# Performance work log

Hardware: AMD Instinct MI355X
Metric: run time of the kernel (lower is better)

The kernel has to match this reference:

```python
import jax, jax.numpy as jnp
import numpy as np

SPANS = [15, 9, 5]   # processed largest-first, matching sorted(span_groups, reverse=True)
DEPTH = 2
TOL = 1.5


def _rmsnorm(x, eps=1e-5):
    return x * jax.lax.rsqrt(jnp.mean(x * x, axis=-1, keepdims=True) + eps)


def _block(m, g, Wi, Wz, Wdt, bdt, alog, Wo, Wyg):
    """Dual-input gated selective-scan block (stand-in for create_multihead_block
    block_type='dual_input'): match stream runs a diagonal SSM scan over window
    tokens, gated by the geometry stream; both streams are residually updated."""
    u = _rmsnorm(m) @ Wi                              # [P,L,C]
    z = jax.nn.silu(_rmsnorm(g) @ Wz)                 # [P,L,C] geom gate
    delta = jax.nn.softplus(u @ Wdt + bdt)            # [P,L,C]
    decay = jnp.exp(delta * (-jnp.exp(alog)))         # [P,L,C]
    x_in = delta * u

    def step(h, inp):
        d, xi = inp
        h = d * h + xi
        return h, h

    _, hs = jax.lax.scan(step, jnp.zeros_like(x_in[:, 0]),
                         (jnp.swapaxes(decay, 0, 1), jnp.swapaxes(x_in, 0, 1)))
    y = jnp.swapaxes(hs, 0, 1) * z                    # [P,L,C]
    return m + y @ Wo, g + jax.nn.silu(y @ Wyg)


def _sample(feat_flat, ys, xs, H, W):
    """Bilinear sampling, align_corners=True, padding_mode='zeros'.
    feat_flat: [C, H*W]; ys, xs: [L] float coords. Returns [L, C]."""
    y0 = jnp.floor(ys); x0 = jnp.floor(xs)
    wy = ys - y0; wx = xs - x0

    def tap(yi, xi):
        valid = ((yi >= 0) & (yi <= H - 1) & (xi >= 0) & (xi <= W - 1)).astype(feat_flat.dtype)
        idx = (jnp.clip(yi, 0, H - 1).astype(jnp.int32) * W
               + jnp.clip(xi, 0, W - 1).astype(jnp.int32))
        return feat_flat[:, idx] * valid              # [C,L]

    v = (tap(y0, x0) * (1 - wy) * (1 - wx) + tap(y0, x0 + 1) * (1 - wy) * wx
         + tap(y0 + 1, x0) * wy * (1 - wx) + tap(y0 + 1, x0 + 1) * wy * wx)
    return v.T


def _process_side(feat_m, feat_g, flow, sx, sy, params):
    B, C, H, W = feat_m.shape
    G = feat_g.shape[1]
    Wi, Wz, Wdt, bdt, alog, Wo, Wyg = params
    dt = feat_m.dtype
    bb, yy, xx = [a.ravel() for a in jnp.meshgrid(jnp.arange(B), jnp.arange(H), jnp.arange(W), indexing='ij')]
    # flow-shifted sub-pixel window centers, clamped (flow[...,0]=dx, flow[...,1]=dy)
    cy = jnp.clip(yy.astype(dt) + flow[bb, yy, xx, 1], 0, H - 1)
    cx = jnp.clip(xx.astype(dt) + flow[bb, yy, xx, 0], 0, W - 1)
    avg = ((sx + sy) * 0.5).ravel()
    assigned = jnp.zeros(avg.shape, dtype=bool)
    fm = feat_m.reshape(B, C, H * W)
    fg = feat_g.reshape(B, G, H * W)
    out_m = jnp.zeros((B * H * W, C), dt)
    out_g = jnp.zeros((B * H * W, G), dt)
    wsum = jnp.zeros((B * H * W,), dt)
    for si, s in enumerate(SPANS):
        # span-group mask; positions claimed by a larger span are excluded
        mask = (jnp.abs(avg - s) < TOL) & (~assigned)
        assigned = assigned | mask
        h = s // 2
        dy, dx = [a.ravel() for a in jnp.meshgrid(jnp.arange(-h, h + 1), jnp.arange(-h, h + 1), indexing='ij')]
        dist = jnp.sqrt((dy * dy + dx * dx).astype(dt))
        pw = jnp.exp(-dist / (s / 2.0))
        pw = pw / pw.sum()                             # normalized distance weights [L]
        ys = cy[:, None] + dy[None, :].astype(dt)      # [P,L]
        xs = cx[:, None] + dx[None, :].astype(dt)
        wm = jax.vmap(lambda b, y, x: _sample(fm[b], y, x, H, W))(bb, ys, xs)  # [P,L,C]
        wg = jax.vmap(lambda b, y, x: _sample(fg[b], y, x, H, W))(bb, ys, xs)  # [P,L,G]
        for d in range(DEPTH):
            wm, wg = _block(wm, wg, Wi[si, d], Wz[si, d], Wdt[si, d], bdt[si, d], alog[si, d], Wo[si, d], Wyg[si, d])
        # scatter-accumulate around the integer center position
        ty = yy[:, None] + dy[None, :]
        tx = xx[:, None] + dx[None, :]
        valid = ((ty >= 0) & (ty < H) & (tx >= 0) & (tx < W)).astype(dt)
        w = pw[None, :] * mask[:, None].astype(dt) * valid           # [P,L]
        idx = bb[:, None] * (H * W) + jnp.clip(ty, 0, H - 1) * W + jnp.clip(tx, 0, W - 1)
        out_m = out_m.at[idx.ravel()].add((wm * w[..., None]).reshape(-1, C))
        out_g = out_g.at[idx.ravel()].add((wg * w[..., None]).reshape(-1, G))
        wsum = wsum.at[idx.ravel()].add(w.ravel())
    ws = jnp.maximum(wsum, 1e-6)[:, None]
    om = (out_m / ws).reshape(B, H, W, C).transpose(0, 3, 1, 2)
    og = (out_g / ws).reshape(B, H, W, G).transpose(0, 3, 1, 2)
    return om, og


def setup_inputs() -> dict:
    key = jax.random.key(0)
    ks = jax.random.split(key, 18)
    B, C, G, H, W = 1, 128, 64, 28, 28
    f32 = jnp.float32
    d = {}
    d['feat_match_0'] = jax.random.normal(ks[0], (B, C, H, W), f32)
    d['feat_match_1'] = jax.random.normal(ks[1], (B, C, H, W), f32)
    d['feat_geom_0'] = jax.random.normal(ks[2], (B, G, H, W), f32)
    d['feat_geom_1'] = jax.random.normal(ks[3], (B, G, H, W), f32)
    d['flow_map_0'] = 1.5 * jax.random.normal(ks[4], (B, H, W, 4), f32)
    d['flow_map_1'] = 1.5 * jax.random.normal(ks[5], (B, H, W, 4), f32)
    # spans in [3, 17) so each span group {5, 9, 15} is populated
    d['adaptive_spans_x_0'] = 3.0 + 14.0 * jax.random.uniform(ks[6], (B, H, W), f32)
    d['adaptive_spans_y_0'] = 3.0 + 14.0 * jax.random.uniform(ks[7], (B, H, W), f32)
    d['adaptive_spans_x_1'] = 3.0 + 14.0 * jax.random.uniform(ks[8], (B, H, W), f32)
    d['adaptive_spans_y_1'] = 3.0 + 14.0 * jax.random.uniform(ks[9], (B, H, W), f32)
    # per-span (order [15,9,5]) x per-depth block parameters
    d['W_in'] = jax.random.normal(ks[10], (3, DEPTH, C, C), f32) / np.sqrt(C).astype(np.float32)
    d['W_z'] = jax.random.normal(ks[11], (3, DEPTH, G, C), f32) / np.sqrt(G).astype(np.float32)
    d['W_dt'] = jax.random.normal(ks[12], (3, DEPTH, C, C), f32) / np.sqrt(C).astype(np.float32)
    d['b_dt'] = 0.1 * jax.random.normal(ks[13], (3, DEPTH, C), f32)
    d['a_log'] = 0.1 * jax.random.normal(ks[14], (3, DEPTH, C), f32)
    d['W_out'] = jax.random.normal(ks[15], (3, DEPTH, C, C), f32) / np.sqrt(C).astype(np.float32)
    d['W_yg'] = jax.random.normal(ks[16], (3, DEPTH, C, G), f32) / np.sqrt(C).astype(np.float32)
    return d


def reference(feat_match_0, feat_match_1, feat_geom_0, feat_geom_1,
              flow_map_0, flow_map_1,
              adaptive_spans_x_0, adaptive_spans_y_0,
              adaptive_spans_x_1, adaptive_spans_y_1,
              W_in, W_z, W_dt, b_dt, a_log, W_out, W_yg):
    params = (W_in, W_z, W_dt, b_dt, a_log, W_out, W_yg)
    m0, g0 = _process_side(feat_match_0, feat_geom_0, flow_map_0[..., :2],
                           adaptive_spans_x_0, adaptive_spans_y_0, params)
    m1, g1 = _process_side(feat_match_1, feat_geom_1, flow_map_1[..., :2],
                           adaptive_spans_x_1, adaptive_spans_y_1, params)
    return m0, m1, g0, g1
```

## Files before the change

### kernel.cpp

```cpp
#include <hip/hip_runtime.h>
#include <math.h>

typedef short s16x8 __attribute__((ext_vector_type(8)));
typedef unsigned short u16x8v __attribute__((ext_vector_type(8)));
typedef float f32x4 __attribute__((ext_vector_type(4)));

#define HH 28
#define WW 28
#define PP 784
#define CC 128
#define GG 64
#define MT 48
#define NH 3
#define AST 136
#define GSTB 72

#define OFF_FMT0 0
#define OFF_FMT1 100352
#define OFF_FGT0 200704
#define OFF_FGT1 250880
#define OFF_ACCM0 301056
#define OFF_ACCM1 401408
#define OFF_ACCG0 501760
#define OFF_ACCG1 551936
#define OFF_ACCW0 602112
#define OFF_ACCW1 602896
#define ACC_FLOATS 302624
#define OFF_CNT   603680
#define OFF_CNT2  603704
#define OFF_JOB   603728
#define OFF_WB    605296

#define WIB 0
#define WZB 98304
#define WDB 147456
#define WOB 245760
#define WYB 344064

struct KArgs {
  const float* fm[2]; const float* fg[2];
  const float* flow[2]; const float* sx[2]; const float* sy[2];
  const float* Wi; const float* Wz; const float* Wdt; const float* bdt;
  const float* alog; const float* Wo; const float* Wyg;
  float* fmT[2]; float* fgT[2];
  float* accm[2]; float* accg[2]; float* accw[2];
  int* cnt; int* cnt2; int* job;
  unsigned short* wb;
  float* out;
};

__device__ __forceinline__ int span_group(float avg, int& s) {
  if (fabsf(avg - 15.f) < 1.5f) { s = 15; return 0; }
  if (fabsf(avg - 9.f)  < 1.5f) { s = 9;  return 1; }
  if (fabsf(avg - 5.f)  < 1.5f) { s = 5;  return 2; }
  s = 0; return 3;
}

__device__ __forceinline__ float fast_silu(float x) {
  return x * __builtin_amdgcn_rcpf(1.f + __expf(-x));
}

__device__ __forceinline__ unsigned short f2bf(float f) {
  unsigned u = __float_as_uint(f);
  unsigned r = (u + 0x7fffu + ((u >> 16) & 1u)) >> 16;
  return (unsigned short)r;
}
__device__ __forceinline__ float b2f(unsigned short u) {
  return __uint_as_float(((unsigned)u) << 16);
}

#define MFMA(A_, B_, C_) __builtin_amdgcn_mfma_f32_16x16x32_bf16((A_), (B_), (C_), 0, 0, 0)

__global__ void k_zero(float* p, int n) {
  int j = blockIdx.x * 256 + threadIdx.x;
  if (j < n) p[j] = 0.f;
}

__global__ void k_prep(KArgs a) {
  int j = blockIdx.x * 256 + threadIdx.x;
  int side = j / 150528; int r = j - side * 150528;
  int p = r / 192; int ch = r - p * 192;
  if (ch < CC) a.fmT[side][p * CC + ch] = a.fm[side][ch * PP + p];
  else         a.fgT[side][p * GG + (ch - CC)] = a.fg[side][(ch - CC) * PP + p];
}

__global__ void k_prepw(KArgs a) {
  int j = blockIdx.x * 256 + threadIdx.x;
  unsigned short* wb = a.wb;
  if (j < 98304) {
    int set = j >> 14, r = j & 16383; int o = r >> 7, c = r & 127;
    wb[WIB + j] = f2bf(a.Wi[set * 16384 + c * 128 + o]);
  } else if (j < 147456) {
    int r = j - 98304; int set = r >> 13, rr = r & 8191; int o = rr >> 6, c = rr & 63;
    wb[WZB + r] = f2bf(a.Wz[set * 8192 + c * 128 + o]);
  } else if (j < 245760) {
  } else if (j < 344064) {
    int r = j - 245760; int set = r >> 14, rr = r & 16383; int o = rr >> 7, c = rr & 127;
    wb[WOB + r] = f2bf(a.Wo[set * 16384 + c * 128 + o]);
  } else {
    int r = j - 344064; int set = r >> 13, rr = r & 8191; int o = rr >> 7, c = rr & 127;
    wb[WYB + r] = f2bf(a.Wyg[set * 8192 + c * 64 + o]);
  }
}

__global__ void k_prepwid(KArgs a) {
  __shared__ float wi_row[128];
  const int set = blockIdx.x, i = blockIdx.y, o = threadIdx.x;
  wi_row[o] = a.Wi[set * 16384 + i * 128 + o];
  __syncthreads();
  float acc = 0.f;
#pragma unroll 4
  for (int m = 0; m < 128; ++m) acc = fmaf(wi_row[m], a.Wdt[set * 16384 + m * 128 + o], acc);
  a.wb[WDB + set * 16384 + o * 128 + i] = f2bf(acc);
}

__global__ void k_count(KArgs a) {
  int j = blockIdx.x * 256 + threadIdx.x;
  if (j >= 2 * PP) return;
  a.job[j] = -1;
  int side = j / PP, p = j - side * PP;
  float avg = 0.5f * (a.sx[side][p] + a.sy[side][p]);
  int s; int g = span_group(avg, s);
  if (g < 3) {
    int py = p / WW, px = p - py * WW;
    int region = (py / 14) * 4 + px / 7;
    atomicAdd(&a.cnt[region * 3 + g], 1);
  }
}

__global__ void k_assign(KArgs a) {
  int j = blockIdx.x * 256 + threadIdx.x;
  if (j >= 2 * PP) return;
  int side = j / PP, p = j - side * PP;
  float avg = 0.5f * (a.sx[side][p] + a.sy[side][p]);
  int s; int g = span_group(avg, s);
  if (g < 3) {
    int py = p / WW, px = p - py * WW;
    int region = (py / 14) * 4 + px / 7;
    int base = 0;
    for (int gg = 0; gg < g; ++gg) base += a.cnt[region * 3 + gg];
    int rank = base + atomicAdd(&a.cnt2[region * 3 + g], 1);
    a.job[region + 8 * rank] = (side << 10) | p;
  }
}

__global__ void k_fin(KArgs a) {
  int j = blockIdx.x * 256 + threadIdx.x;
  int side = j / 150528; int r = j - side * 150528;
  int p = r / 192; int ch = r - p * 192;
  float inv = 1.f / fmaxf(a.accw[side][p], 1e-6f);
  if (ch < CC) a.out[side * 100352 + ch * PP + p] = a.accm[side][p * CC + ch] * inv;
  else         a.out[200704 + side * 50176 + (ch - CC) * PP + p] = a.accg[side][p * GG + (ch - CC)] * inv;
}

__launch_bounds__(256, 2)
__global__ void k_main(KArgs a) {
  __shared__ __align__(16) unsigned short mres[2][MT * AST];
  __shared__ __align__(16) unsigned short gres[2][MT * GSTB];
  __shared__ __align__(16) unsigned short bufA[MT * AST];
  __shared__ __align__(16) unsigned short bufB[MT * GSTB];
  __shared__ float hs[2 * CC];
  __shared__ float na_s[2 * CC];
  __shared__ float bb_s[2 * CC];
  __shared__ float pw_l[228];
  __shared__ int   tap_i[MT * 4];
  __shared__ float tap_w[MT * 4];
  __shared__ int   sc_i[2][MT];
  __shared__ float sc_w[2][MT];
  __shared__ float red[4];

  const int tid = threadIdx.x;
  const int job = a.job[blockIdx.x];
  if (job < 0) return;
  const int side = job >> 10, p = job & 1023;
  const float avg = 0.5f * (a.sx[side][p] + a.sy[side][p]);
  int s; const int si = span_group(avg, s);
  const int hspan = s >> 1, L = s * s;
  const int py = p / WW, px = p - py * WW;
  const float fdx = a.flow[side][p * 4 + 0], fdy = a.flow[side][p * 4 + 1];
  const float cy = fminf(fmaxf((float)py + fdy, 0.f), (float)(HH - 1));
  const float cx = fminf(fmaxf((float)px + fdx, 0.f), (float)(WW - 1));
  const float* fmT = a.fmT[side]; const float* fgT = a.fgT[side];
  float* accm = a.accm[side]; float* accg = a.accg[side]; float* accw = a.accw[side];

  const unsigned short* wb = a.wb;
  const int wv = tid >> 6, l = tid & 63, lm = l & 15, g = l >> 4;
  const int o0 = 32 * wv + lm, o1 = o0 + 16, og = 16 * wv + lm;
  const int ttk = tid >> 3, c8 = tid & 7;

  { const int d2 = tid >> 7, c2 = tid & 127;
    na_s[tid] = -__expf(a.alog[(si * 2 + d2) * CC + c2]);
    bb_s[tid] = a.bdt[(si * 2 + d2) * CC + c2];
    hs[tid] = 0.f; }
  if (tid < L) {
    const int dyi = tid / s - hspan, dxi = tid % s - hspan;
    pw_l[tid] = __expf(-sqrtf((float)(dyi * dyi + dxi * dxi)) / (0.5f * (float)s));
  }
  __syncthreads();
  { float v = (tid < L) ? pw_l[tid] : 0.f;
#pragma unroll
    for (int off = 32; off > 0; off >>= 1) v += __shfl_xor(v, off);
    if ((tid & 63) == 0) red[tid >> 6] = v; }
  __syncthreads();
  { const float pinv = 1.f / (red[0] + red[1] + red[2] + red[3]);
    if (tid < L) pw_l[tid] *= pinv; }
  __syncthreads();

  auto comp_taps = [&](int t0_, int b_) {
    if (tid < MT) {
      const int t = t0_ + tid;
      if (t < L) {
        const int tq = t / s;
        const int dyi = tq - hspan, dxi = (t - tq * s) - hspan;
        const float ys = cy + (float)dyi, xs = cx + (float)dxi;
        const float y0f = floorf(ys), x0f = floorf(xs);
        const float wy = ys - y0f, wx = xs - x0f;
        const int y0 = (int)y0f, x0 = (int)x0f;
#pragma unroll
        for (int k = 0; k < 4; ++k) {
          const int yi = y0 + (k >> 1), xi = x0 + (k & 1);
          const bool v = (yi >= 0) && (yi < HH) && (xi >= 0) && (xi < WW);
          const int yc = min(max(yi, 0), HH - 1), xc = min(max(xi, 0), WW - 1);
          tap_i[tid * 4 + k] = yc * WW + xc;
          const float wgt = ((k >> 1) ? wy : 1.f - wy) * ((k & 1) ? wx : 1.f - wx);
          tap_w[tid * 4 + k] = v ? wgt : 0.f;
        }
        const int ty = py + dyi, tx = px + dxi;
        const bool sv = (ty >= 0) && (ty < HH) && (tx >= 0) && (tx < WW);
        const int sid2 = sv ? ty * WW + tx : 0;
        const float sw = sv ? pw_l[t] : 0.f;
        sc_i[b_][tid] = sid2; sc_w[b_][tid] = sw;
        if (sw != 0.f) atomicAdd(&accw[sid2], sw);
      } else {
#pragma unroll
        for (int k = 0; k < 4; ++k) { tap_i[tid * 4 + k] = 0; tap_w[tid * 4 + k] = 0.f; }
        sc_i[b_][tid] = 0; sc_w[b_][tid] = 0.f;
      }
    }
  };

  auto sample_tile = [&](int b_) {
    for (int tk = ttk; tk < MT; tk += 32) {
      const int* ti = &tap_i[tk * 4]; const float* tw = &tap_w[tk * 4];
      f32x4 am0 = {0.f,0.f,0.f,0.f}, am1 = am0, am2 = am0, am3 = am0;
      f32x4 ag0 = am0, ag1 = am0;
#pragma unroll
      for (int k2 = 0; k2 < 4; ++k2) {
        const float w = tw[k2];
        const float* pm = &fmT[ti[k2] * CC + c8 * 16];
        am0 += w * *(const f32x4*)&pm[0];
        am1 += w * *(const f32x4*)&pm[4];
        am2 += w * *(const f32x4*)&pm[8];
        am3 += w * *(const f32x4*)&pm[12];
        const float* pg = &fgT[ti[k2] * GG + c8 * 8];
        ag0 += w * *(const f32x4*)&pg[0];
        ag1 += w * *(const f32x4*)&pg[4];
      }
      u16x8v w0, w1, wg;
#pragma unroll
      for (int j = 0; j < 4; ++j) {
        w0[j] = f2bf(am0[j]); w0[4 + j] = f2bf(am1[j]);
        w1[j] = f2bf(am2[j]); w1[4 + j] = f2bf(am3[j]);
        wg[j] = f2bf(ag0[j]); wg[4 + j] = f2bf(ag1[j]);
      }
      *(u16x8v*)&mres[b_][tk * AST + c8 * 16] = w0;
      *(u16x8v*)&mres[b_][tk * AST + c8 * 16 + 8] = w1;
      *(u16x8v*)&gres[b_][tk * GSTB + c8 * 8] = wg;
    }
  };

  const int nt = (L + MT - 1) / MT;
  comp_taps(0, 0);
  __syncthreads();
  sample_tile(0);
  int cur = 0;

  for (int t = 0; t < nt; ++t) {
    const int t0 = t * MT;
    const int tlen = min(MT, L - t0);
    const int nxt = cur ^ 1;
    __syncthreads();
    if (t + 1 < nt) comp_taps(t0 + MT, nxt);

    for (int d = 0; d < 2; ++d) {
      const unsigned short* Wib  = wb + WIB + (si * 2 + d) * 16384;
      const unsigned short* Widb = wb + WDB + (si * 2 + d) * 16384;
      const unsigned short* Wzb  = wb + WZB + (si * 2 + d) * 8192;
      const unsigned short* Wob  = wb + WOB + (si * 2 + d) * 16384;
      const unsigned short* Wyb  = wb + WYB + (si * 2 + d) * 8192;
      if (d == 1) __syncthreads();
      for (int tk = ttk; tk < MT; tk += 32) {
        u16x8v m0 = *(const u16x8v*)&mres[cur][tk * AST + c8 * 16];
        u16x8v m1 = *(const u16x8v*)&mres[cur][tk * AST + c8 * 16 + 8];
        u16x8v gv = *(const u16x8v*)&gres[cur][tk * GSTB + c8 * 8];
        float mv[16], gvf[8];
#pragma unroll
        for (int k = 0; k < 8; ++k) { mv[k] = b2f(m0[k]); mv[8 + k] = b2f(m1[k]); gvf[k] = b2f(gv[k]); }
        float ssm = 0.f, ssg = 0.f;
#pragma unroll
        for (int k = 0; k < 16; ++k) ssm = fmaf(mv[k], mv[k], ssm);
#pragma unroll
        for (int k = 0; k < 8; ++k) ssg = fmaf(gvf[k], gvf[k], ssg);
#pragma unroll
        for (int off = 4; off > 0; off >>= 1) { ssm += __shfl_xor(ssm, off); ssg += __shfl_xor(ssg, off); }
        const float sm = rsqrtf(ssm * (1.f / CC) + 1e-5f);
        const float sgs = rsqrtf(ssg * (1.f / GG) + 1e-5f);
        u16x8v xa, xb, gx;
#pragma unroll
        for (int k = 0; k < 8; ++k) { xa[k] = f2bf(mv[k] * sm); xb[k] = f2bf(mv[8 + k] * sm); gx[k] = f2bf(gvf[k] * sgs); }
        *(u16x8v*)&bufA[tk * AST + c8 * 16] = xa;
        *(u16x8v*)&bufA[tk * AST + c8 * 16 + 8] = xb;
        *(u16x8v*)&bufB[tk * GSTB + c8 * 8] = gx;
      }
      __syncthreads();
      f32x4 u[NH][2], dt[NH][2], z[NH][2];
#pragma unroll
      for (int h = 0; h < NH; ++h)
#pragma unroll
        for (int j2 = 0; j2 < 2; ++j2) { u[h][j2] = (f32x4){0.f,0.f,0.f,0.f}; dt[h][j2] = (f32x4){0.f,0.f,0.f,0.f}; z[h][j2] = (f32x4){0.f,0.f,0.f,0.f}; }
#pragma unroll
      for (int h = 0; h < NH; ++h) {
        const int ar = (h * 16 + lm) * AST, gr = (h * 16 + lm) * GSTB;
#pragma unroll
        for (int ss = 0; ss < 4; ++ss) {
          const int c0 = 32 * ss + g * 8;
          s16x8 av = *(const s16x8*)&bufA[ar + c0];
          u[h][0]  = MFMA(av, *(const s16x8*)&Wib[o0 * 128 + c0], u[h][0]);
          u[h][1]  = MFMA(av, *(const s16x8*)&Wib[o1 * 128 + c0], u[h][1]);
          dt[h][0] = MFMA(av, *(const s16x8*)&Widb[o0 * 128 + c0], dt[h][0]);
          dt[h][1] = MFMA(av, *(const s16x8*)&Widb[o1 * 128 + c0], dt[h][1]);
        }
#pragma unroll
        for (int ss = 0; ss < 2; ++ss) {
          const int c0 = 32 * ss + g * 8;
          s16x8 gv2 = *(const s16x8*)&bufB[gr + c0];
          z[h][0] = MFMA(gv2, *(const s16x8*)&Wzb[o0 * 64 + c0], z[h][0]);
          z[h][1] = MFMA(gv2, *(const s16x8*)&Wzb[o1 * 64 + c0], z[h][1]);
        }
      }
#pragma unroll
      for (int h = 0; h < NH; ++h)
#pragma unroll
        for (int j2 = 0; j2 < 2; ++j2)
#pragma unroll
          for (int r = 0; r < 4; ++r) z[h][j2][r] = fast_silu(z[h][j2][r]);

#pragma unroll
      for (int j2 = 0; j2 < 2; ++j2) {
        const int oc = j2 ? o1 : o0;
        const float bb = bb_s[d * CC + oc], na = na_s[d * CC + oc];
        float hcar = hs[d * CC + oc];
#pragma unroll
        for (int h = 0; h < NH; ++h) {
          float Pl[4], Dl[4]; float P = 0.f, D = 1.f;
#pragma unroll
          for (int r = 0; r < 4; ++r) {
            const float x = dt[h][j2][r] + bb;
            float dlt = fmaxf(x, 0.f) + __logf(1.f + __expf(-fabsf(x)));
            float dec = __expf(dlt * na), xin = dlt * u[h][j2][r];
            if (h * 16 + 4 * g + r >= tlen) { dec = 1.f; xin = 0.f; }
            P = dec * P + xin; D *= dec; Pl[r] = P; Dl[r] = D;
          }
          float Pi = P, Di = D;
          { float pa = __shfl_up(Pi, 16), da = __shfl_up(Di, 16);
            if (g >= 1) { Pi = Di * pa + Pi; Di *= da; }
            pa = __shfl_up(Pi, 32); da = __shfl_up(Di, 32);
            if (g >= 2) { Pi = Di * pa + Pi; Di *= da; } }
          float Pe = __shfl_up(Pi, 16), De = __shfl_up(Di, 16);
          if (g == 0) { Pe = 0.f; De = 1.f; }
          const float cr = De * hcar + Pe;
          const float Pf = __shfl(Pi, 48 + lm), Df = __shfl(Di, 48 + lm);
#pragma unroll
          for (int r = 0; r < 4; ++r) z[h][j2][r] = (Dl[r] * cr + Pl[r]) * z[h][j2][r];
          hcar = Df * hcar + Pf;
        }
        if (g == 0) hs[d * CC + oc] = hcar;
      }
      __syncthreads();
#pragma unroll
      for (int h = 0; h < NH; ++h)
#pragma unroll
        for (int r = 0; r < 4; ++r) {
          const int rw = h * 16 + 4 * g + r;
          bufA[rw * AST + o0] = f2bf(z[h][0][r]);
          bufA[rw * AST + o1] = f2bf(z[h][1][r]);
        }
      __syncthreads();
      if (d == 0 && t + 1 < nt) sample_tile(nxt);
      f32x4 dm[NH][2], dgv[NH];
#pragma unroll
      for (int h = 0; h < NH; ++h) { dm[h][0] = (f32x4){0.f,0.f,0.f,0.f}; dm[h][1] = (f32x4){0.f,0.f,0.f,0.f}; dgv[h] = (f32x4){0.f,0.f,0.f,0.f}; }
#pragma unroll
      for (int h = 0; h < NH; ++h) {
        const int ar = (h * 16 + lm) * AST;
#pragma unroll
        for (int ss = 0; ss < 4; ++ss) {
          const int c0 = 32 * ss + g * 8;
          s16x8 av = *(const s16x8*)&bufA[ar + c0];
          dm[h][0] = MFMA(av, *(const s16x8*)&Wob[o0 * 128 + c0], dm[h][0]);
          dm[h][1] = MFMA(av, *(const s16x8*)&Wob[o1 * 128 + c0], dm[h][1]);
          dgv[h]   = MFMA(av, *(const s16x8*)&Wyb[og * 128 + c0], dgv[h]);
        }
      }
#pragma unroll
      for (int h = 0; h < NH; ++h)
#pragma unroll
        for (int r = 0; r < 4; ++r) {
          const int rw = h * 16 + 4 * g + r;
          mres[cur][rw * AST + o0] = f2bf(b2f(mres[cur][rw * AST + o0]) + dm[h][0][r]);
          mres[cur][rw * AST + o1] = f2bf(b2f(mres[cur][rw * AST + o1]) + dm[h][1][r]);
          gres[cur][rw * GSTB + og] = f2bf(b2f(gres[cur][rw * GSTB + og]) + fast_silu(dgv[h][r]));
        }
    }
    __syncthreads();

    for (int j = tid; j < tlen * 192; j += 256) {
      const int tt = j / 192, ch = j - tt * 192;
      const float w = sc_w[cur][tt];
      if (w != 0.f) {
        const int tgt = sc_i[cur][tt];
        if (ch < CC) atomicAdd(&accm[tgt * CC + ch], b2f(mres[cur][tt * AST + ch]) * w);
        else         atomicAdd(&accg[tgt * GG + (ch - CC)], b2f(gres[cur][tt * GSTB + (ch - CC)]) * w);
      }
    }
    cur = nxt;
  }
}

extern "C" void kernel_launch(void* const* d_in, const int* in_sizes, int n_in,
                              void* d_out, int out_size, void* d_ws, size_t ws_size,
                              hipStream_t stream) {
  (void)in_sizes; (void)n_in; (void)out_size; (void)ws_size;
  float* ws = (float*)d_ws;
  KArgs a;
  a.fm[0]  = (const float*)d_in[0]; a.fm[1]  = (const float*)d_in[1];
  a.fg[0]  = (const float*)d_in[2]; a.fg[1]  = (const float*)d_in[3];
  a.flow[0] = (const float*)d_in[4]; a.flow[1] = (const float*)d_in[5];
  a.sx[0] = (const float*)d_in[6]; a.sy[0] = (const float*)d_in[7];
  a.sx[1] = (const float*)d_in[8]; a.sy[1] = (const float*)d_in[9];
  a.Wi  = (const float*)d_in[10]; a.Wz   = (const float*)d_in[11];
  a.Wdt = (const float*)d_in[12]; a.bdt  = (const float*)d_in[13];
  a.alog = (const float*)d_in[14]; a.Wo  = (const float*)d_in[15];
  a.Wyg = (const float*)d_in[16];
  a.fmT[0] = ws + OFF_FMT0; a.fmT[1] = ws + OFF_FMT1;
  a.fgT[0] = ws + OFF_FGT0; a.fgT[1] = ws + OFF_FGT1;
  a.accm[0] = ws + OFF_ACCM0; a.accm[1] = ws + OFF_ACCM1;
  a.accg[0] = ws + OFF_ACCG0; a.accg[1] = ws + OFF_ACCG1;
  a.accw[0] = ws + OFF_ACCW0; a.accw[1] = ws + OFF_ACCW1;
  a.cnt  = (int*)(ws + OFF_CNT);
  a.cnt2 = (int*)(ws + OFF_CNT2);
  a.job  = (int*)(ws + OFF_JOB);
  a.wb   = (unsigned short*)(ws + OFF_WB);
  a.out = (float*)d_out;

  k_zero<<<1183, 256, 0, stream>>>(ws + OFF_ACCM0, ACC_FLOATS);
  k_zero<<<1, 256, 0, stream>>>(ws + OFF_CNT, 48);
  k_prep<<<1176, 256, 0, stream>>>(a);
  k_prepw<<<1536, 256, 0, stream>>>(a);
  k_prepwid<<<dim3(6, 128), 128, 0, stream>>>(a);
  k_count<<<7, 256, 0, stream>>>(a);
  k_assign<<<7, 256, 0, stream>>>(a);
  k_main<<<1568, 256, 0, stream>>>(a);
  k_fin<<<1176, 256, 0, stream>>>(a);
}
```

Measured before the change: 232.8 us.

## Fuse final residual scatter into MFMA epilogue with packed fp16 atomics

On the last depth, the residual update and weighted scatter-add now happen directly in the MFMA epilogue instead of writing back to shared memory and doing a separate atomic pass. Neighbouring lanes are paired with shuffles so that each issues one packed two-wide fp16 atomic add, halving the number of global atomics. The accumulators become fp16, and the final kernel reads them back as fp16. This reduces atomic traffic and a sync and shared-memory pass, but fp16 accumulation of many contributions risks precision loss or overflow. It also depends on the accumulator zeroing and layout matching the new half-width reinterpretation.

```diff
diff --git a/kernel.cpp b/kernel.cpp
--- a/kernel.cpp
+++ b/kernel.cpp
@@ -4,6 +4,7 @@
 typedef short s16x8 __attribute__((ext_vector_type(8)));
 typedef unsigned short u16x8v __attribute__((ext_vector_type(8)));
 typedef float f32x4 __attribute__((ext_vector_type(4)));
+typedef _Float16 h2 __attribute__((ext_vector_type(2)));
 
 #define HH 28
 #define WW 28
@@ -67,6 +68,22 @@
 }
 __device__ __forceinline__ float b2f(unsigned short u) {
   return __uint_as_float(((unsigned)u) << 16);
+}
+
+__device__ __forceinline__ void atomic_pk2(_Float16* base, float x, float y) {
+  h2 v; v[0] = (_Float16)x; v[1] = (_Float16)y;
+#if __has_builtin(__builtin_amdgcn_global_atomic_fadd_v2f16)
+  __builtin_amdgcn_global_atomic_fadd_v2f16((h2*)base, v);
+#else
+  unsigned* a = (unsigned*)base;
+  unsigned old = *a, assumed;
+  do {
+    assumed = old;
+    h2 cur = *(h2*)&assumed;
+    h2 nw; nw[0] = cur[0] + v[0]; nw[1] = cur[1] + v[1];
+    old = atomicCAS(a, assumed, *(unsigned*)&nw);
+  } while (old != assumed);
+#endif
 }
 
 #define MFMA(A_, B_, C_) __builtin_amdgcn_mfma_f32_16x16x32_bf16((A_), (B_), (C_), 0, 0, 0)
@@ -149,8 +166,13 @@
   int side = j / 150528; int r = j - side * 150528;
   int p = r / 192; int ch = r - p * 192;
   float inv = 1.f / fmaxf(a.accw[side][p], 1e-6f);
-  if (ch < CC) a.out[side * 100352 + ch * PP + p] = a.accm[side][p * CC + ch] * inv;
-  else         a.out[200704 + side * 50176 + (ch - CC) * PP + p] = a.accg[side][p * GG + (ch - CC)] * inv;
+  if (ch < CC) {
+    const _Float16* amh = (const _Float16*)a.accm[side];
+    a.out[side * 100352 + ch * PP + p] = (float)amh[p * CC + ch] * inv;
+  } else {
+    const _Float16* agh = (const _Float16*)a.accg[side];
+    a.out[200704 + side * 50176 + (ch - CC) * PP + p] = (float)agh[p * GG + (ch - CC)] * inv;
+  }
 }
 
 __launch_bounds__(256, 2)
@@ -181,7 +203,9 @@
   const float cy = fminf(fmaxf((float)py + fdy, 0.f), (float)(HH - 1));
   const float cx = fminf(fmaxf((float)px + fdx, 0.f), (float)(WW - 1));
   const float* fmT = a.fmT[side]; const float* fgT = a.fgT[side];
-  float* accm = a.accm[side]; float* accg = a.accg[side]; float* accw = a.accw[side];
+  _Float16* accm_h = (_Float16*)a.accm[side];
+  _Float16* accg_h = (_Float16*)a.accg[side];
+  float* accw = a.accw[side];
 
   const unsigned short* wb = a.wb;
   const int wv = tid >> 6, l = tid & 63, lm = l & 15, g = l >> 4;
@@ -402,25 +426,40 @@
           dgv[h]   = MFMA(av, *(const s16x8*)&Wyb[og * 128 + c0], dgv[h]);
         }
       }
-#pragma unroll
-      for (int h = 0; h < NH; ++h)
-#pragma unroll
-        for (int r = 0; r < 4; ++r) {
-          const int rw = h * 16 + 4 * g + r;
-          mres[cur][rw * AST + o0] = f2bf(b2f(mres[cur][rw * AST + o0]) + dm[h][0][r]);
-          mres[cur][rw * AST + o1] = f2bf(b2f(mres[cur][rw * AST + o1]) + dm[h][1][r]);
-          gres[cur][rw * GSTB + og] = f2bf(b2f(gres[cur][rw * GSTB + og]) + fast_silu(dgv[h][r]));
-        }
-    }
-    __syncthreads();
-
-    for (int j = tid; j < tlen * 192; j += 256) {
-      const int tt = j / 192, ch = j - tt * 192;
-      const float w = sc_w[cur][tt];
-      if (w != 0.f) {
-        const int tgt = sc_i[cur][tt];
-        if (ch < CC) atomicAdd(&accm[tgt * CC + ch], b2f(mres[cur][tt * AST + ch]) * w);
-        else         atomicAdd(&accg[tgt * GG + (ch - CC)], b2f(gres[cur][tt * GSTB + (ch - CC)]) * w);
+      if (d == 0) {
+#pragma unroll
+        for (int h = 0; h < NH; ++h)
+#pragma unroll
+          for (int r = 0; r < 4; ++r) {
+            const int rw = h * 16 + 4 * g + r;
+            mres[cur][rw * AST + o0] = f2bf(b2f(mres[cur][rw * AST + o0]) + dm[h][0][r]);
+            mres[cur][rw * AST + o1] = f2bf(b2f(mres[cur][rw * AST + o1]) + dm[h][1][r]);
+            gres[cur][rw * GSTB + og] = f2bf(b2f(gres[cur][rw * GSTB + og]) + fast_silu(dgv[h][r]));
+          }
+      } else {
+        const bool evn = (lm & 1) == 0;
+#pragma unroll
+        for (int h = 0; h < NH; ++h)
+#pragma unroll
+          for (int r = 0; r < 4; ++r) {
+            const int rw = h * 16 + 4 * g + r;
+            const float w = sc_w[cur][rw];
+            const int tgt = sc_i[cur][rw];
+            const float vm0 = (b2f(mres[cur][rw * AST + o0]) + dm[h][0][r]) * w;
+            const float vm1 = (b2f(mres[cur][rw * AST + o1]) + dm[h][1][r]) * w;
+            const float vg  = (b2f(gres[cur][rw * GSTB + og]) + fast_silu(dgv[h][r])) * w;
+            const float pm0 = __shfl_xor(vm0, 1);
+            const float pm1 = __shfl_xor(vm1, 1);
+            const float pg  = __shfl_xor(vg, 1);
+            if (w != 0.f) {
+              if (evn) {
+                atomic_pk2(accm_h + tgt * CC + o0, vm0, pm0);
+                atomic_pk2(accg_h + tgt * GG + og, vg, pg);
+              } else {
+                atomic_pk2(accm_h + tgt * CC + o1 - 1, pm1, vm1);
+              }
+            }
+          }
       }
     }
     cur = nxt;
```

Result: faster. 212.0 us (-8.9%).
